# Optimization experiments

Hardware: AMD Instinct MI355X
Metric: run time of the kernel (lower is better)

The kernel has to match this reference:

```python
import jax, jax.numpy as jnp
import numpy as np

N = 100000      # number of nodes
E = 1600000     # number of (directed) edges, avg degree 16
DIN = 128       # in_features
DOUT = 32       # out_features
SLOPE = 0.2     # leaky relu negative slope


def setup_inputs() -> dict:
    key = jax.random.key(0)
    k1, k2, k3, k4, k5, k6 = jax.random.split(key, 6)
    x = jax.random.normal(k1, (N, DIN), dtype=jnp.float32)
    edge_index = jax.random.randint(k2, (2, E), 0, N, dtype=jnp.int32)
    # W1 (shared with W2 and used as the feature-update matrix W, 'source' mode)
    W1_w = jax.random.normal(k3, (DOUT, DIN), dtype=jnp.float32) / np.float32(np.sqrt(DIN))
    W1_b = jax.random.normal(k4, (DOUT,), dtype=jnp.float32) * 0.01
    a1_w = jax.random.normal(k5, (DOUT,), dtype=jnp.float32) / np.float32(np.sqrt(DOUT))
    a2_w = jax.random.normal(k6, (DOUT,), dtype=jnp.float32) / np.float32(np.sqrt(DOUT))
    return {"x": x, "edge_index": edge_index, "W1_w": W1_w, "W1_b": W1_b,
            "a1_w": a1_w, "a2_w": a2_w}


def reference(x, edge_index, W1_w, W1_b, a1_w, a2_w):
    n = x.shape[0]
    # append self-loops, as in _sparse_attention
    loops = jnp.arange(n, dtype=edge_index.dtype)
    src = jnp.concatenate([edge_index[0], loops])   # rows  (softmax segments)
    dst = jnp.concatenate([edge_index[1], loops])   # cols
    # h = W1(x) (linear, with bias); W2 = W1 (weight sharing), W = W2 ('source')
    h = x @ W1_w.T + W1_b                           # [N, DOUT]
    z = jax.nn.leaky_relu(h, SLOPE)                 # x1 == x2 under weight sharing
    s1 = z @ a1_w                                   # [N] per-node src score
    s2 = z @ a2_w                                   # [N] per-node dst score
    logits = s1[src] + s2[dst]                      # [E+N] per-edge attention logit
    # row-wise (dim=1) sparse softmax == segment softmax over src
    m = jax.ops.segment_max(logits, src, num_segments=n)
    ex = jnp.exp(logits - m[src])
    denom = jax.ops.segment_sum(ex, src, num_segments=n)
    alpha = ex / denom[src]                         # normalized attention per edge
    # sparse-dense matmul: out[i] = sum_{(i,j)} alpha_ij * h[j]
    return jax.ops.segment_sum(alpha[:, None] * h[dst], src, num_segments=n)
```

## Files before the change

### kernel.cpp

```cpp
#include <hip/hip_runtime.h>
#include <hip/hip_fp16.h>

#define DIN 128
#define DOUT 32
#define SLOPE 0.2f

#define BSHIFT 7
#define BNODES 128
#define NBS    1024
#define BPITCH 784
#define CAP    3072
#define TILE   4096
#define EPB    (TILE / 256)

typedef short s16x8 __attribute__((ext_vector_type(8)));
typedef float f32x4 __attribute__((ext_vector_type(4)));

__device__ __forceinline__ short f2bf(float f) {
    unsigned u = __float_as_uint(f);
    return (short)((u + 0x7fffu + ((u >> 16) & 1u)) >> 16);
}
__device__ __forceinline__ float bf2f(short s) {
    return __uint_as_float(((unsigned)(unsigned short)s) << 16);
}

__device__ __forceinline__ void linear_role(
    int tile, int ntiles, int lane, int N,
    const float* __restrict__ x, const float* __restrict__ W,
    const float* __restrict__ b, const float* __restrict__ a2,
    __half* __restrict__ g16, float* __restrict__ es2)
{
    if (tile >= ntiles) return;
    int m = lane & 15, oct = lane >> 4;
    long rowbase = (long)tile * 16;

    s16x8 bh[2][4], bl[2][4];
    #pragma unroll
    for (int t = 0; t < 2; ++t) {
        const float* wrow = W + (long)(t * 16 + m) * DIN + oct * 8;
        #pragma unroll
        for (int kc = 0; kc < 4; ++kc) {
            float4 w0 = *(const float4*)(wrow + kc * 32);
            float4 w1 = *(const float4*)(wrow + kc * 32 + 4);
            float wf[8] = {w0.x, w0.y, w0.z, w0.w, w1.x, w1.y, w1.z, w1.w};
            #pragma unroll
            for (int j = 0; j < 8; ++j) {
                short hh = f2bf(wf[j]);
                bh[t][kc][j] = hh;
                bl[t][kc][j] = f2bf(wf[j] - bf2f(hh));
            }
        }
    }

    long lrow = rowbase + m; if (lrow > N - 1) lrow = N - 1;
    const float* xrow = x + lrow * DIN + oct * 8;
    f32x4 acc0 = {0.f, 0.f, 0.f, 0.f}, acc1 = {0.f, 0.f, 0.f, 0.f};
    #pragma unroll
    for (int kc = 0; kc < 4; ++kc) {
        float4 x0 = *(const float4*)(xrow + kc * 32);
        float4 x1 = *(const float4*)(xrow + kc * 32 + 4);
        float xf[8] = {x0.x, x0.y, x0.z, x0.w, x1.x, x1.y, x1.z, x1.w};
        s16x8 ah, al;
        #pragma unroll
        for (int j = 0; j < 8; ++j) {
            short hh = f2bf(xf[j]);
            ah[j] = hh;
            al[j] = f2bf(xf[j] - bf2f(hh));
        }
        acc0 = __builtin_amdgcn_mfma_f32_16x16x32_bf16(al, bh[0][kc], acc0, 0, 0, 0);
        acc0 = __builtin_amdgcn_mfma_f32_16x16x32_bf16(ah, bl[0][kc], acc0, 0, 0, 0);
        acc0 = __builtin_amdgcn_mfma_f32_16x16x32_bf16(ah, bh[0][kc], acc0, 0, 0, 0);
        acc1 = __builtin_amdgcn_mfma_f32_16x16x32_bf16(al, bh[1][kc], acc1, 0, 0, 0);
        acc1 = __builtin_amdgcn_mfma_f32_16x16x32_bf16(ah, bl[1][kc], acc1, 0, 0, 0);
        acc1 = __builtin_amdgcn_mfma_f32_16x16x32_bf16(ah, bh[1][kc], acc1, 0, 0, 0);
    }

    int c0 = m, c1 = 16 + m;
    float b0 = b[c0], b1 = b[c1], A0 = a2[c0], A1 = a2[c1];
    float hv0[4], hv1[4], sp[4];
    #pragma unroll
    for (int i = 0; i < 4; ++i) {
        hv0[i] = acc0[i] + b0;
        hv1[i] = acc1[i] + b1;
        float z0 = hv0[i] > 0.f ? hv0[i] : SLOPE * hv0[i];
        float z1 = hv1[i] > 0.f ? hv1[i] : SLOPE * hv1[i];
        sp[i] = z0 * A0 + z1 * A1;
    }
    #pragma unroll
    for (int off = 1; off <= 8; off <<= 1) {
        #pragma unroll
        for (int i = 0; i < 4; ++i) sp[i] += __shfl_xor(sp[i], off, 64);
    }
    #pragma unroll
    for (int i = 0; i < 4; ++i) {
        long r = rowbase + oct * 4 + i;
        if (r >= N) continue;
        float ev = __expf(sp[i]);
        g16[r * DOUT + c0] = __float2half(ev * hv0[i]);
        g16[r * DOUT + c1] = __float2half(ev * hv1[i]);
        if (m == 0) es2[r] = ev;
    }
}

__global__ __launch_bounds__(256) void gat_fused(
    const float* __restrict__ x, const float* __restrict__ W,
    const float* __restrict__ b, const float* __restrict__ a2,
    const int* __restrict__ src, const int* __restrict__ dst,
    __half* __restrict__ g16, float* __restrict__ es2,
    unsigned* __restrict__ ebuf, int* __restrict__ boff,
    int N, int E, int ntiles, int nbin)
{
    if ((int)blockIdx.x >= nbin) {
        int wave = threadIdx.x >> 6;
        int tile = (blockIdx.x - nbin) * 4 + wave;
        linear_role(tile, ntiles, threadIdx.x & 63, N, x, W, b, a2, g16, es2);
        return;
    }
    __shared__ int cnt[NBS];
    __shared__ int offs[NBS];
    __shared__ int wsum[4], wbase[4];
    int tid = threadIdx.x;
    long tstart = (long)blockIdx.x * TILE;

    for (int i = tid; i < NBS; i += 256) cnt[i] = 0;
    __syncthreads();

    unsigned rec[EPB];
    int      bq[EPB];
    #pragma unroll
    for (int it = 0; it < EPB; ++it) {
        long e = tstart + it * 256 + tid;
        int s = (e < E) ? src[e] : -1;
        int d = (e < E) ? dst[e] : 0;
        if (s >= 0) {
            int bk = s >> BSHIFT;
            int rv = atomicAdd(&cnt[bk], 1);
            rec[it] = ((unsigned)(s & (BNODES - 1)) << 17) | (unsigned)d;
            bq[it] = (rv < 511) ? ((bk << 9) | rv) : -1;
        } else bq[it] = -1;
    }
    __syncthreads();

    int t4 = tid << 2;
    int c0 = cnt[t4], c1 = cnt[t4 + 1], c2 = cnt[t4 + 2], c3 = cnt[t4 + 3];
    int s4 = c0 + c1 + c2 + c3;
    int v = s4;
    #pragma unroll
    for (int off = 1; off < 64; off <<= 1) {
        int t = __shfl_up(v, off, 64);
        if ((tid & 63) >= off) v += t;
    }
    if ((tid & 63) == 63) wsum[tid >> 6] = v;
    __syncthreads();
    if (tid == 0) {
        int a = 0;
        #pragma unroll
        for (int w = 0; w < 4; ++w) { wbase[w] = a; a += wsum[w]; }
    }
    __syncthreads();
    int base = wbase[tid >> 6] + (v - s4);
    offs[t4]     = base;
    offs[t4 + 1] = base + c0;
    offs[t4 + 2] = base + c0 + c1;
    offs[t4 + 3] = base + c0 + c1 + c2;
    __syncthreads();

    for (int i = tid; i < BPITCH - 1; i += 256)
        boff[(size_t)blockIdx.x * BPITCH + i] = offs[i];
    if (tid == 0)
        boff[(size_t)blockIdx.x * BPITCH + BPITCH - 1] = offs[BPITCH - 1];

    #pragma unroll
    for (int it = 0; it < EPB; ++it) {
        int q = bq[it];
        if (q >= 0) {
            int pos = offs[q >> 9] + (q & 511);
            ebuf[tstart + pos] = rec[it];
        }
    }
}

__global__ __launch_bounds__(512) void gat_aggregate(
    const __half* __restrict__ g16, const float* __restrict__ es2,
    const unsigned* __restrict__ ebuf, const int* __restrict__ boff,
    float* __restrict__ out, int N, int nbin)
{
    __shared__ unsigned rs[CAP];
    __shared__ unsigned srt[CAP];
    __shared__ int cnt[BNODES];
    __shared__ int sc[BNODES];
    __shared__ int basep[BNODES];
    __shared__ int pos2[BNODES];
    __shared__ int wsum[8], wbase[8], totsh;
    int tid = threadIdx.x;
    int bk = blockIdx.x;

    if (tid < BNODES) { cnt[tid] = 0; pos2[tid] = 0; }
    __syncthreads();

    int rstart = 0, rlen = 0;
    if (tid < nbin) {
        const int* row = boff + (size_t)tid * BPITCH;
        rstart = row[bk];
        rlen   = row[bk + 1] - rstart;
    }
    int v = rlen;
    #pragma unroll
    for (int off = 1; off < 64; off <<= 1) {
        int t = __shfl_up(v, off, 64);
        if ((tid & 63) >= off) v += t;
    }
    if ((tid & 63) == 63) wsum[tid >> 6] = v;
    __syncthreads();
    if (tid == 0) {
        int a = 0;
        #pragma unroll
        for (int w = 0; w < 8; ++w) { wbase[w] = a; a += wsum[w]; }
        totsh = a;
    }
    __syncthreads();
    int dest = wbase[tid >> 6] + (v - rlen);
    int lim = CAP - dest; if (lim < 0) lim = 0;
    if (rlen > lim) rlen = lim;
    {
        const unsigned* seg = ebuf + (size_t)tid * TILE + rstart;
        for (int j = 0; j < rlen; ++j) {
            unsigned u = seg[j];
            rs[dest + j] = u;
            atomicAdd(&cnt[u >> 17], 1);
        }
    }
    __syncthreads();
    int cntb = totsh; if (cntb > CAP) cntb = CAP;

    if (tid < BNODES) sc[tid] = cnt[tid];
    __syncthreads();
    #pragma unroll
    for (int off = 1; off < BNODES; off <<= 1) {
        int t = (tid >= off && tid < BNODES) ? sc[tid - off] : 0;
        __syncthreads();
        if (tid < BNODES) sc[tid] += t;
        __syncthreads();
    }
    if (tid < BNODES) basep[tid] = sc[tid] - cnt[tid];
    __syncthreads();
    for (int r = tid; r < cntb; r += 512) {
        unsigned u = rs[r];
        int sl = (int)(u >> 17);
        int p = basep[sl] + atomicAdd(&pos2[sl], 1);
        srt[p] = u & 0x1FFFFu;
    }
    __syncthreads();

    int unit = tid >> 5, col = tid & 31;
    for (int sl = unit; sl < BNODES; sl += 16) {
        long node = (long)bk * BNODES + sl;
        if (node >= N) break;
        float acc = __half2float(g16[node * DOUT + col]);
        float d = es2[node];
        int e = basep[sl], e_end = basep[sl] + cnt[sl];

        while (e + 8 <= e_end) {
            int dn[8];
            #pragma unroll
            for (int j = 0; j < 8; ++j) dn[j] = (int)srt[e + j];
            unsigned short gv[8];
            #pragma unroll
            for (int j = 0; j < 8; ++j)
                gv[j] = *(const unsigned short*)&g16[(long)dn[j] * DOUT + col];
            float ev[8];
            #pragma unroll
            for (int j = 0; j < 8; ++j) ev[j] = es2[dn[j]];
            #pragma unroll
            for (int j = 0; j < 8; ++j) {
                acc += __half2float(*(const __half*)&gv[j]);
                d += ev[j];
            }
            e += 8;
        }
        while (e + 4 <= e_end) {
            int dn[4];
            #pragma unroll
            for (int j = 0; j < 4; ++j) dn[j] = (int)srt[e + j];
            unsigned short gv[4];
            #pragma unroll
            for (int j = 0; j < 4; ++j)
                gv[j] = *(const unsigned short*)&g16[(long)dn[j] * DOUT + col];
            float ev[4];
            #pragma unroll
            for (int j = 0; j < 4; ++j) ev[j] = es2[dn[j]];
            #pragma unroll
            for (int j = 0; j < 4; ++j) {
                acc += __half2float(*(const __half*)&gv[j]);
                d += ev[j];
            }
            e += 4;
        }
        for (; e < e_end; ++e) {
            int dn = (int)srt[e];
            acc += __half2float(g16[(long)dn * DOUT + col]);
            d += es2[dn];
        }
        out[node * DOUT + col] = acc / d;
    }
}

extern "C" void kernel_launch(void* const* d_in, const int* in_sizes, int n_in,
                              void* d_out, int out_size, void* d_ws, size_t ws_size,
                              hipStream_t stream)
{
    const float* x  = (const float*)d_in[0];
    const int*   ei = (const int*)d_in[1];
    const float* W  = (const float*)d_in[2];
    const float* b  = (const float*)d_in[3];
    const float* a2 = (const float*)d_in[5];
    float* out = (float*)d_out;

    int N = in_sizes[0] / DIN;
    int E = in_sizes[1] / 2;
    const int* src = ei;
    const int* dst = ei + E;

    int NB = (N + BNODES - 1) >> BSHIFT;
    int nbin = (E + TILE - 1) / TILE;

    char* ws = (char*)d_ws;
    __half*   g16  = (__half*)ws;   ws += (size_t)N * DOUT * sizeof(__half);
    float*    es2  = (float*)ws;    ws += (size_t)N * sizeof(float);
    int*      boff = (int*)ws;      ws += (size_t)nbin * BPITCH * sizeof(int);
    unsigned* ebuf = (unsigned*)ws; ws += (size_t)nbin * TILE * sizeof(unsigned);

    int ntiles = (N + 15) / 16;
    int nlin   = (ntiles + 3) / 4;

    gat_fused    <<<nbin + nlin, 256, 0, stream>>>(x, W, b, a2, src, dst,
                                                   g16, es2, ebuf, boff,
                                                   N, E, ntiles, nbin);
    gat_aggregate<<<NB, 512, 0, stream>>>(g16, es2, ebuf, boff, out, N, nbin);
}
```

Baseline: 165.7 us.

## Replace per-bin counting sort with LDS atomic accumulation and XCD-aware block remap

The aggregate kernel no longer counting-sorts each bin's edges by local node in shared memory. Instead each 32-lane unit takes an equal slice of the unsorted edge list and atomically adds gathered features and exp-scores into shared per-node accumulators. This removes the histogram, the scan with its many barriers, and the scatter pass, and evens out the work per unit, at the cost of LDS float atomic contention and non-deterministic summation order. Block indices are also remapped so that consecutive bins land on the same XCD, for L2 locality.

```diff
diff --git a/kernel.cpp b/kernel.cpp
--- a/kernel.cpp
+++ b/kernel.cpp
@@ -186,23 +186,25 @@
     float* __restrict__ out, int N, int nbin)
 {
     __shared__ unsigned rs[CAP];
-    __shared__ unsigned srt[CAP];
-    __shared__ int cnt[BNODES];
-    __shared__ int sc[BNODES];
-    __shared__ int basep[BNODES];
-    __shared__ int pos2[BNODES];
+    __shared__ float acc[BNODES][DOUT];
+    __shared__ float den[BNODES];
     __shared__ int wsum[8], wbase[8], totsh;
     int tid = threadIdx.x;
-    int bk = blockIdx.x;
-
-    if (tid < BNODES) { cnt[tid] = 0; pos2[tid] = 0; }
-    __syncthreads();
+
+    int nwg = gridDim.x;
+    int xcd = blockIdx.x & 7;
+    int q = nwg >> 3, rr = nwg & 7;
+    int bk = (xcd < rr ? xcd * (q + 1) : rr * (q + 1) + (xcd - rr) * q)
+           + ((int)blockIdx.x >> 3);
+
+    for (int i = tid; i < BNODES * DOUT; i += 512) ((float*)acc)[i] = 0.f;
+    if (tid < BNODES) den[tid] = 0.f;
 
     int rstart = 0, rlen = 0;
     if (tid < nbin) {
-        const int* row = boff + (size_t)tid * BPITCH;
-        rstart = row[bk];
-        rlen   = row[bk + 1] - rstart;
+        const int* row = boff + (size_t)tid * BPITCH + bk;
+        rstart = row[0];
+        rlen   = row[1] - rstart;
     }
     int v = rlen;
     #pragma unroll
@@ -224,84 +226,60 @@
     if (rlen > lim) rlen = lim;
     {
         const unsigned* seg = ebuf + (size_t)tid * TILE + rstart;
-        for (int j = 0; j < rlen; ++j) {
-            unsigned u = seg[j];
-            rs[dest + j] = u;
-            atomicAdd(&cnt[u >> 17], 1);
-        }
+        for (int j = 0; j < rlen; ++j)
+            rs[dest + j] = seg[j];
     }
     __syncthreads();
     int cntb = totsh; if (cntb > CAP) cntb = CAP;
 
-    if (tid < BNODES) sc[tid] = cnt[tid];
-    __syncthreads();
-    #pragma unroll
-    for (int off = 1; off < BNODES; off <<= 1) {
-        int t = (tid >= off && tid < BNODES) ? sc[tid - off] : 0;
-        __syncthreads();
-        if (tid < BNODES) sc[tid] += t;
-        __syncthreads();
-    }
-    if (tid < BNODES) basep[tid] = sc[tid] - cnt[tid];
-    __syncthreads();
-    for (int r = tid; r < cntb; r += 512) {
-        unsigned u = rs[r];
-        int sl = (int)(u >> 17);
-        int p = basep[sl] + atomicAdd(&pos2[sl], 1);
-        srt[p] = u & 0x1FFFFu;
-    }
-    __syncthreads();
-
     int unit = tid >> 5, col = tid & 31;
+    {
+        int r    = (cntb * unit) >> 4;
+        int rend = (cntb * (unit + 1)) >> 4;
+
+        while (r + 8 <= rend) {
+            unsigned uu[8];
+            #pragma unroll
+            for (int j = 0; j < 8; ++j) uu[j] = rs[r + j];
+            int dn[8], sl[8];
+            #pragma unroll
+            for (int j = 0; j < 8; ++j) { dn[j] = (int)(uu[j] & 0x1FFFFu);
+                                          sl[j] = (int)(uu[j] >> 17); }
+            unsigned short gv[8];
+            #pragma unroll
+            for (int j = 0; j < 8; ++j)
+                gv[j] = *(const unsigned short*)&g16[(long)dn[j] * DOUT + col];
+            float ev[8];
+            if (col == 0) {
+                #pragma unroll
+                for (int j = 0; j < 8; ++j) ev[j] = es2[dn[j]];
+            }
+            #pragma unroll
+            for (int j = 0; j < 8; ++j)
+                unsafeAtomicAdd(&acc[sl[j]][col],
+                                __half2float(*(const __half*)&gv[j]));
+            if (col == 0) {
+                #pragma unroll
+                for (int j = 0; j < 8; ++j) unsafeAtomicAdd(&den[sl[j]], ev[j]);
+            }
+            r += 8;
+        }
+        for (; r < rend; ++r) {
+            unsigned u = rs[r];
+            int dn = (int)(u & 0x1FFFFu), sl = (int)(u >> 17);
+            unsafeAtomicAdd(&acc[sl][col],
+                            __half2float(g16[(long)dn * DOUT + col]));
+            if (col == 0) unsafeAtomicAdd(&den[sl], es2[dn]);
+        }
+    }
+    __syncthreads();
+
     for (int sl = unit; sl < BNODES; sl += 16) {
         long node = (long)bk * BNODES + sl;
         if (node >= N) break;
-        float acc = __half2float(g16[node * DOUT + col]);
-        float d = es2[node];
-        int e = basep[sl], e_end = basep[sl] + cnt[sl];
-
-        while (e + 8 <= e_end) {
-            int dn[8];
-            #pragma unroll
-            for (int j = 0; j < 8; ++j) dn[j] = (int)srt[e + j];
-            unsigned short gv[8];
-            #pragma unroll
-            for (int j = 0; j < 8; ++j)
-                gv[j] = *(const unsigned short*)&g16[(long)dn[j] * DOUT + col];
-            float ev[8];
-            #pragma unroll
-            for (int j = 0; j < 8; ++j) ev[j] = es2[dn[j]];
-            #pragma unroll
-            for (int j = 0; j < 8; ++j) {
-                acc += __half2float(*(const __half*)&gv[j]);
-                d += ev[j];
-            }
-            e += 8;
-        }
-        while (e + 4 <= e_end) {
-            int dn[4];
-            #pragma unroll
-            for (int j = 0; j < 4; ++j) dn[j] = (int)srt[e + j];
-            unsigned short gv[4];
-            #pragma unroll
-            for (int j = 0; j < 4; ++j)
-                gv[j] = *(const unsigned short*)&g16[(long)dn[j] * DOUT + col];
-            float ev[4];
-            #pragma unroll
-            for (int j = 0; j < 4; ++j) ev[j] = es2[dn[j]];
-            #pragma unroll
-            for (int j = 0; j < 4; ++j) {
-                acc += __half2float(*(const __half*)&gv[j]);
-                d += ev[j];
-            }
-            e += 4;
-        }
-        for (; e < e_end; ++e) {
-            int dn = (int)srt[e];
-            acc += __half2float(g16[(long)dn * DOUT + col]);
-            d += es2[dn];
-        }
-        out[node * DOUT + col] = acc / d;
+        float self = __half2float(g16[node * DOUT + col]);
+        float dsum = den[sl] + es2[node];
+        out[node * DOUT + col] = (acc[sl][col] + self) / dsum;
     }
 }
 
```

Result: slower. 487.8 us (+194.4%).
